# Optimization experiments

Hardware: AMD Instinct MI355X
Metric: run time of the kernel (lower is better)

Reference implementation:

```python
import jax, jax.numpy as jnp
import numpy as np

B, D, NC = 64, 5, 24          # batch, conv output spatial, conv channels
NCELL = D * D                 # 25 objects
FEAT = NC + 2                 # 26 = channels + 2 coords
QDIM = FEAT * NCELL           # 650
PAIR = FEAT * 2 + QDIM        # 702 = g_fc1 in_features
EPS = 1e-5

# cvt_coord(i) = [(i/5 - 2)/2, (i%5 - 2)/2]  (python3 true division)
_i = np.arange(NCELL, dtype=np.float32)
COORDS = jnp.asarray(np.stack([(_i / 5.0 - 2.0) / 2.0, (_i % 5.0 - 2.0) / 2.0], axis=1))  # [25,2]


def _conv_bn(x, w, b, g, beta):
    # Conv2d(stride=2, padding=1) -> ReLU -> BatchNorm2d (training-mode batch stats)
    y = jax.lax.conv_general_dilated(x, w, (2, 2), [(1, 1), (1, 1)],
                                     dimension_numbers=('NCHW', 'OIHW', 'NCHW'))
    y = jax.nn.relu(y + b[None, :, None, None])
    m = y.mean(axis=(0, 2, 3), keepdims=True)
    v = y.var(axis=(0, 2, 3), keepdims=True)  # biased, as torch BN
    return (y - m) * jax.lax.rsqrt(v + EPS) * g[None, :, None, None] + beta[None, :, None, None]


def _cnn(x, conv_w1, conv_w234, conv_b, bn_g, bn_b):
    y = _conv_bn(x, conv_w1, conv_b[0], bn_g[0], bn_b[0])
    for i in range(3):
        y = _conv_bn(y, conv_w234[i], conv_b[i + 1], bn_g[i + 1], bn_b[i + 1])
    return y  # [B,24,5,5]


def setup_inputs() -> dict:
    key = jax.random.key(0)
    ks = jax.random.split(key, 20)
    s = 0.05
    return {
        'img':  jax.random.normal(ks[0], (B, 3, 80, 80), jnp.float32),
        'img2': jax.random.normal(ks[1], (B, 3, 80, 80), jnp.float32),
        'conv_w1':   jax.random.normal(ks[2], (NC, 3, 3, 3), jnp.float32) * s,
        'conv_w234': jax.random.normal(ks[3], (3, NC, NC, 3, 3), jnp.float32) * s,
        'conv_b': jax.random.normal(ks[4], (4, NC), jnp.float32) * s,
        'bn_g':   1.0 + jax.random.normal(ks[5], (4, NC), jnp.float32) * s,
        'bn_b':   jax.random.normal(ks[6], (4, NC), jnp.float32) * s,
        'g_w1':   jax.random.normal(ks[7], (256, PAIR), jnp.float32) * s,
        'g_w234': jax.random.normal(ks[8], (3, 256, 256), jnp.float32) * s,
        'g_b':    jax.random.normal(ks[9], (4, 256), jnp.float32) * s,
        'f_w1':  jax.random.normal(ks[10], (256, 256), jnp.float32) * s,
        'f_b1':  jax.random.normal(ks[11], (256,), jnp.float32) * s,
        'fc2_w': jax.random.normal(ks[12], (256, 256), jnp.float32) * s,
        'fc2_b': jax.random.normal(ks[13], (256,), jnp.float32) * s,
        'fc3_w': jax.random.normal(ks[14], (128, 256), jnp.float32) * s,
        'fc3_b': jax.random.normal(ks[15], (128,), jnp.float32) * s,
    }


def reference(img, img2, conv_w1, conv_w234, conv_b, bn_g, bn_b,
              g_w1, g_w234, g_b, f_w1, f_b1, fc2_w, fc2_b, fc3_w, fc3_b):
    x = _cnn(img, conv_w1, conv_w234, conv_b, bn_g, bn_b)
    x2 = _cnn(img2, conv_w1, conv_w234, conv_b, bn_g, bn_b)

    # [B,24,25] -> [B,25,24] -> concat coords -> [B,25,26]
    coords = jnp.broadcast_to(COORDS[None], (B, NCELL, 2))
    feat = jnp.concatenate([x.reshape(B, NC, NCELL).transpose(0, 2, 1), coords], axis=2)
    feat2 = jnp.concatenate([x2.reshape(B, NC, NCELL).transpose(0, 2, 1), coords], axis=2)
    qst = feat2.reshape(B, QDIM)  # [B,650]

    # x_full[b,a,c] = cat(feat[b,c], feat[b,a], qst[b])  -> [B,25,25,702]
    pair = jnp.concatenate([
        jnp.broadcast_to(feat[:, None, :, :], (B, NCELL, NCELL, FEAT)),
        jnp.broadcast_to(feat[:, :, None, :], (B, NCELL, NCELL, FEAT)),
        jnp.broadcast_to(qst[:, None, None, :], (B, NCELL, NCELL, QDIM)),
    ], axis=-1)

    h = pair.reshape(B * NCELL * NCELL, PAIR)
    h = jax.nn.relu(h @ g_w1.T + g_b[0])
    for i in range(3):
        h = jax.nn.relu(h @ g_w234[i].T + g_b[i + 1])

    x_g = h.reshape(B, NCELL * NCELL, 256).sum(axis=1)  # sum pooling over 625 pairs

    x_f = jax.nn.relu(x_g @ f_w1.T + f_b1)
    y = jax.nn.relu(x_f @ fc2_w.T + fc2_b)
    # F.dropout is identity here (deterministic reference / eval mode)
    y = y @ fc3_w.T + fc3_b                 # [B,128]
    y = jax.nn.softmax(y.reshape(B, 16, 8), axis=2)
    y = jnp.clip(y, 0.001, jnp.max(y))
    return y.reshape(B, 128)
```

## Files before the change

kernel.cpp:

```cpp
#include <hip/hip_runtime.h>

typedef short bf16x8 __attribute__((ext_vector_type(8)));
typedef float f32x4  __attribute__((ext_vector_type(4)));

#define EPSF 1e-5f

#define OFF_P0   0
#define OFF_U    1048576
#define OFF_V    1572864
#define OFF_P1   4915200
#define OFF_SS   6144000
#define OFF_SACC 6144384
#define OFF_Q    6144512
#define OFF_WP   6160896
#define OFF_W1UV 6357504
#define OFF_W1Q  6370816
#define OFF_FW1T 6537216
#define OFF_FC2T 6602752
#define OFF_FC3T 6668288
#define OFF_XG   6701056

__device__ __forceinline__ unsigned short f2bf(float f) {
    union { float f; unsigned u; } cv; cv.f = f;
    const unsigned u = cv.u;
    return (unsigned short)((u + 0x7fffu + ((u >> 16) & 1u)) >> 16);
}
__device__ __forceinline__ float bf2f(unsigned short h) {
    union { unsigned u; float f; } cv; cv.u = (unsigned)h << 16; return cv.f;
}

__global__ __launch_bounds__(256) void k_prep(
    const float* __restrict__ gw1, const float* __restrict__ gw234,
    const float* __restrict__ fw1, const float* __restrict__ fc2w,
    const float* __restrict__ fc3w, float* __restrict__ ws)
{
    int idx = blockIdx.x * 256 + threadIdx.x;
    if (idx < 16384) { ws[OFF_XG + idx] = 0.f; return; }
    idx -= 16384;
    if (idx < 384) {
        if (idx < 96) ws[OFF_SACC + idx] = 0.f;
        else          ws[OFF_U + (idx - 96)] = 0.f;
        return;
    }
    idx -= 384;
    if (idx < 49152) {
        const int isLo = idx >= 24576;
        const int f = isLo ? idx - 24576 : idx;
        const int lane = f & 63;
        const int nt = (f >> 6) & 15;
        const int kb = (f >> 10) & 7;
        const int l  = f >> 13;
        const int o = nt * 16 + (lane & 15);
        const int k = kb * 32 + (lane >> 4) * 8;
        const float* src = gw234 + ((size_t)l * 256 + o) * 256 + k;
        unsigned short* dst = (unsigned short*)(ws + OFF_WP) + (size_t)idx * 8;
        #pragma unroll
        for (int j = 0; j < 8; ++j) {
            const float x = src[j];
            const unsigned short hi = f2bf(x);
            dst[j] = isLo ? f2bf(x - bf2f(hi)) : hi;
        }
        return;
    }
    idx -= 49152;
    if (idx < 13312) {
        const int o = idx & 255, k = idx >> 8;
        ws[OFF_W1UV + idx] = gw1[(size_t)o * 702 + k];
        return;
    }
    idx -= 13312;
    if (idx < 166400) {
        const int o = idx & 255, k = idx >> 8;
        ws[OFF_W1Q + idx] = gw1[(size_t)o * 702 + 52 + k];
        return;
    }
    idx -= 166400;
    if (idx < 65536) { const int o = idx & 255, k = idx >> 8; ws[OFF_FW1T + idx] = fw1[o * 256 + k];  return; }
    idx -= 65536;
    if (idx < 65536) { const int o = idx & 255, k = idx >> 8; ws[OFF_FC2T + idx] = fc2w[o * 256 + k]; return; }
    idx -= 65536;
    if (idx < 32768) { const int o = idx & 127, k = idx >> 7; ws[OFF_FC3T + idx] = fc3w[o * 256 + k]; return; }
}

__global__ __launch_bounds__(256) void k_convF(
    const float* __restrict__ img, const float* __restrict__ img2,
    const float* __restrict__ w, const float* __restrict__ bias,
    float* __restrict__ out, float* __restrict__ sacc)
{
    __shared__ float lds[3*17*82 + 648 + 24];
    __shared__ float lstat[48];
    float* lin   = lds;
    float* lw    = lds + 3*17*82;
    float* lbias = lw + 648;

    const int b  = blockIdx.x / 5;
    const int ty = blockIdx.x % 5;
    const int oy0 = ty * 8;
    const int t = threadIdx.x;

    for (int i = t; i < 648; i += 256) {
        const int co = i % 24, tap = (i / 24) % 9, ci = i / 216;
        lw[i] = w[(co*3 + ci)*9 + tap];
    }
    if (t < 24) lbias[t] = bias[t];
    if (t >= 64 && t < 112) lstat[t - 64] = 0.f;

    const float* src = (b < 64 ? img : img2) + (size_t)(b & 63) * 3 * 6400;
    for (int i = t; i < 3*17*82; i += 256) {
        const int ci = i / (17*82);
        const int r  = i % (17*82);
        const int y  = r / 82, x = r % 82;
        const int gy = 2*oy0 - 1 + y, gx = x - 1;
        float v = 0.f;
        if (gy >= 0 && gy < 80 && gx >= 0 && gx < 80)
            v = src[ci*6400 + gy*80 + gx];
        lin[i] = v;
    }
    __syncthreads();

    const int NWI = 8 * 20 * 24;
    for (int wk = t; wk < NWI; wk += 256) {
        const int co = wk % 24;
        const int pr = wk / 24;
        const int i2 = (pr % 20) * 2;
        const int j  = pr / 20;
        float sA = lbias[co], sB = sA;
        const float* wp = lw + co;
        #pragma unroll
        for (int ci = 0; ci < 3; ++ci) {
            const int base = (ci*17 + 2*j)*82 + 2*i2;
            const float* wc = wp + ci * 216;
            #pragma unroll
            for (int kh = 0; kh < 3; ++kh) {
                const float* lr = lin + base + kh*82;
                const float2 fa = *(const float2*)lr;
                const float2 fb = *(const float2*)(lr + 2);
                const float  fc = lr[4];
                const float w0 = wc[(kh*3 + 0)*24];
                const float w1 = wc[(kh*3 + 1)*24];
                const float w2 = wc[(kh*3 + 2)*24];
                sA += fa.x*w0 + fa.y*w1 + fb.x*w2;
                sB += fb.x*w0 + fb.y*w1 + fc  *w2;
            }
        }
        const float vA = fmaxf(sA, 0.f), vB = fmaxf(sB, 0.f);
        const size_t o = (((size_t)b*24 + co)*40 + oy0 + j)*40 + i2;
        out[o]     = vA;
        out[o + 1] = vB;
        atomicAdd(&lstat[co],      vA + vB);
        atomicAdd(&lstat[24 + co], vA*vA + vB*vB);
    }
    __syncthreads();
    if (t < 48) {
        const int img_i = b >> 6, c = t % 24;
        const int dst = (t < 24) ? (img_i*24 + c) : (48 + img_i*24 + c);
        atomicAdd(&sacc[dst], lstat[t]);
    }
}

__device__ __forceinline__ void convL_body(
    const float* __restrict__ in, const float* __restrict__ ss,
    const float* __restrict__ w, const float* __restrict__ bias,
    float* __restrict__ out, float* __restrict__ sacc,
    float* lds, const int IH, const int IW, const int OH, const int OW,
    const int TH, const int nty)
{
    const int NR = 2*TH + 1, CSTR = IW + 2;
    float* lin = lds;
    float* lw  = lds + 5040;

    const int b  = blockIdx.x / nty;
    const int ty = blockIdx.x % nty;
    const int oy0 = ty * TH;
    const int t = threadIdx.x;

    for (int i = t; i < 5184; i += 256) {
        const int co = i % 24, tap = (i / 24) % 9, ci = i / 216;
        lw[i] = w[(co*24 + ci)*9 + tap];
    }

    const float* sc = ss + (b >> 6) * 48;
    for (int i = t; i < 24 * NR * CSTR; i += 256) {
        const int ci = i / (NR * CSTR);
        const int r  = i % (NR * CSTR);
        const int y  = r / CSTR, x = r % CSTR;
        const int gy = 2*oy0 - 1 + y, gx = x - 1;
        float v = 0.f;
        if (gy >= 0 && gy < IH && gx >= 0 && gx < IW)
            v = in[(((size_t)b*24 + ci)*IH + gy)*IW + gx] * sc[ci] + sc[24 + ci];
        lin[i] = v;
    }
    __syncthreads();

    const int THe = (TH < OH - oy0) ? TH : (OH - oy0);
    const int QPR = (OW + 3) >> 2;
    const int NWI = THe * QPR * 24;
    float ssum = 0.f, ssq = 0.f;
    int myco = 0;
    bool have = false;
    if (t < NWI) {
        const int co = t % 24;
        const int q  = t / 24;
        const int i4 = (q % QPR) * 4;
        const int j  = q / QPR;
        const int n4 = (OW - i4 < 4) ? (OW - i4) : 4;
        float s0 = bias[co], s1 = s0, s2 = s0, s3 = s0;
        const float* wp = lw + co;
        for (int ci = 0; ci < 24; ++ci) {
            const int base = (ci*NR + 2*j)*CSTR + 2*i4;
            const float* wc = wp + ci * 216;
            #pragma unroll
            for (int kh = 0; kh < 3; ++kh) {
                const float* lr = lin + base + kh*CSTR;
                const float2 a0 = *(const float2*)lr;
                const float2 a1 = *(const float2*)(lr + 2);
                const float2 a2 = *(const float2*)(lr + 4);
                const float2 a3 = *(const float2*)(lr + 6);
                const float  a8 = lr[8];
                const float w0 = wc[(kh*3 + 0)*24];
                const float w1 = wc[(kh*3 + 1)*24];
                const float w2 = wc[(kh*3 + 2)*24];
                s0 += a0.x*w0 + a0.y*w1 + a1.x*w2;
                s1 += a1.x*w0 + a1.y*w1 + a2.x*w2;
                s2 += a2.x*w0 + a2.y*w1 + a3.x*w2;
                s3 += a3.x*w0 + a3.y*w1 + a8  *w2;
            }
        }
        const size_t o = (((size_t)b*24 + co)*OH + oy0 + j)*OW + i4;
        const float v0 = fmaxf(s0, 0.f);
        out[o] = v0;  ssum = v0;  ssq = v0*v0;
        if (n4 > 1) { const float v1 = fmaxf(s1, 0.f); out[o+1] = v1; ssum += v1; ssq += v1*v1; }
        if (n4 > 2) { const float v2 = fmaxf(s2, 0.f); out[o+2] = v2; ssum += v2; ssq += v2*v2; }
        if (n4 > 3) { const float v3 = fmaxf(s3, 0.f); out[o+3] = v3; ssum += v3; ssq += v3*v3; }
        myco = co; have = true;
    }
    __syncthreads();
    if (t < 48) lin[t] = 0.f;
    __syncthreads();
    if (have) { atomicAdd(&lin[myco], ssum); atomicAdd(&lin[24 + myco], ssq); }
    __syncthreads();
    if (t < 48) {
        const int img_i = b >> 6, c = t % 24;
        const int dst = (t < 24) ? (img_i*24 + c) : (48 + img_i*24 + c);
        atomicAdd(&sacc[dst], lin[t]);
    }
}

__global__ __launch_bounds__(256) void k_convL2(
    const float* __restrict__ in, const float* __restrict__ ss,
    const float* __restrict__ w, const float* __restrict__ bias,
    float* __restrict__ out, float* __restrict__ sacc)
{
    __shared__ float lds[10224];
    convL_body(in, ss, w, bias, out, sacc, lds, 40, 40, 20, 20, 2, 10);
}
__global__ __launch_bounds__(256) void k_convL3(
    const float* __restrict__ in, const float* __restrict__ ss,
    const float* __restrict__ w, const float* __restrict__ bias,
    float* __restrict__ out, float* __restrict__ sacc)
{
    __shared__ float lds[10224];
    convL_body(in, ss, w, bias, out, sacc, lds, 20, 20, 10, 10, 3, 4);
}
__global__ __launch_bounds__(256) void k_convL4(
    const float* __restrict__ in, const float* __restrict__ ss,
    const float* __restrict__ w, const float* __restrict__ bias,
    float* __restrict__ out, float* __restrict__ sacc)
{
    __shared__ float lds[10224];
    convL_body(in, ss, w, bias, out, sacc, lds, 10, 10, 5, 5, 5, 1);
}

__global__ void k_stats_fin(const float* __restrict__ sacc, const float* __restrict__ g,
                            const float* __restrict__ beta, float* __restrict__ ss, int HW)
{
    const int t = threadIdx.x;
    if (t >= 48) return;
    const int img = t / 24, c = t % 24;
    const float N = 64.f * (float)HW;
    const float mean = sacc[t] / N;
    const float var  = sacc[48 + t] / N - mean*mean;
    const float scale = g[c] * rsqrtf(var + EPSF);
    ss[img*48 + c]      = scale;
    ss[img*48 + 24 + c] = beta[c] - mean * scale;
}

__global__ __launch_bounds__(256) void k_uvq(
    const float* __restrict__ P1, const float* __restrict__ SS4,
    const float* __restrict__ w1uvT, const float* __restrict__ w1qT,
    const float* __restrict__ gb,
    float* __restrict__ Ub, float* __restrict__ Vb, float* __restrict__ Qb)
{
    __shared__ float f[650];
    const int t = threadIdx.x;
    if (blockIdx.x < 1600) {
        const int row = blockIdx.x;
        const int b = row / 25, cell = row % 25;
        if (t < 26) {
            float v;
            if (t < 24)      v = P1[((size_t)(b*24 + t))*25 + cell] * SS4[t] + SS4[24 + t];
            else if (t == 24) v = ((float)cell / 5.f - 2.f) * 0.5f;
            else              v = ((float)(cell % 5) - 2.f) * 0.5f;
            f[t] = v;
        }
        __syncthreads();
        float su = 0.f, sv = 0.f;
        #pragma unroll
        for (int k = 0; k < 26; ++k) {
            su += f[k] * w1uvT[k*256 + t];
            sv += f[k] * w1uvT[(26 + k)*256 + t];
        }
        Ub[(size_t)row*256 + t] = su;
        Vb[(size_t)row*256 + t] = sv;
    } else {
        const int b = blockIdx.x - 1600;
        for (int i = t; i < 650; i += 256) {
            const int cell = i / 26, ff = i % 26;
            float v;
            if (ff < 24)      v = P1[((size_t)((64 + b)*24 + ff))*25 + cell] * SS4[48 + ff] + SS4[72 + ff];
            else if (ff == 24) v = ((float)cell / 5.f - 2.f) * 0.5f;
            else               v = ((float)(cell % 5) - 2.f) * 0.5f;
            f[i] = v;
        }
        __syncthreads();
        float s = gb[t];
        #pragma unroll 10
        for (int k = 0; k < 650; ++k) s += f[k] * w1qT[k*256 + t];
        Qb[b*256 + t] = s;
    }
}

__global__ __launch_bounds__(256, 4) void k_gmlp(
    const float* __restrict__ U, const float* __restrict__ V, const float* __restrict__ Q,
    const unsigned short* __restrict__ WP, const float* __restrict__ gb, float* __restrict__ xg)
{
    __shared__ unsigned short hhi[8192];
    __shared__ unsigned short hlo[8192];
    const int b    = blockIdx.x / 20;
    const int row0 = (blockIdx.x % 20) * 32;
    const int tid  = threadIdx.x;
    const int lane = tid & 63, w = tid >> 6;
    const int w4 = w * 4;

    {
        const int r0 = w * 8;
        const float2* Q2 = (const float2*)(Q + b*256);
        const float2 q0 = Q2[lane], q1 = Q2[64 + lane];
        for (int rr = 0; rr < 8; ++rr) {
            const int row = r0 + rr;
            int p = row0 + row; if (p > 624) p = 624;
            const float2* u2p = (const float2*)(U + ((size_t)(b*25 + p % 25)) * 256);
            const float2* v2p = (const float2*)(V + ((size_t)(b*25 + p / 25)) * 256);
            #pragma unroll
            for (int cc = 0; cc < 2; ++cc) {
                const int cp = cc*64 + lane;
                const float2 u2 = u2p[cp], v2 = v2p[cp];
                const float2 q2 = cc ? q1 : q0;
                const float x0 = fmaxf(u2.x + v2.x + q2.x, 0.f);
                const float x1 = fmaxf(u2.y + v2.y + q2.y, 0.f);
                const unsigned short h0 = f2bf(x0), h1 = f2bf(x1);
                const float l0 = x0 - bf2f(h0), l1 = x1 - bf2f(h1);
                const int byte = (row*512 + cp*4) ^ ((row & 7) << 4);
                *(unsigned*)((char*)hhi + byte) = (unsigned)h0 | ((unsigned)h1 << 16);
                *(unsigned*)((char*)hlo + byte) = (unsigned)f2bf(l0) | ((unsigned)f2bf(l1) << 16);
            }
        }
    }
    __syncthreads();

    const bf16x8* WPB = (const bf16x8*)WP;
    f32x4 acc[2][4];
    #pragma unroll 1
    for (int l = 0; l < 3; ++l) {
        #pragma unroll
        for (int rs = 0; rs < 2; ++rs)
            #pragma unroll
            for (int n = 0; n < 4; ++n) acc[rs][n] = (f32x4)0.f;

        #pragma unroll 1
        for (int kb = 0; kb < 8; ++kb) {
            bf16x8 wh[4], wl[4];
            #pragma unroll
            for (int n = 0; n < 4; ++n) {
                const bf16x8* p = WPB + ((size_t)((l*8 + kb)*16 + w4 + n))*64 + lane;
                wh[n] = p[0]; wl[n] = p[24576];
            }
            bf16x8 ahi[2], alo[2];
            #pragma unroll
            for (int rs = 0; rs < 2; ++rs) {
                const int ar = rs*16 + (lane & 15);
                const int off = (ar*512 + kb*64 + (lane >> 4)*16) ^ ((ar & 7) << 4);
                ahi[rs] = *(const bf16x8*)((char*)hhi + off);
                alo[rs] = *(const bf16x8*)((char*)hlo + off);
            }
            #pragma unroll
            for (int n = 0; n < 4; ++n) {
                #pragma unroll
                for (int rs = 0; rs < 2; ++rs) {
                    acc[rs][n] = __builtin_amdgcn_mfma_f32_16x16x32_bf16(ahi[rs], wh[n], acc[rs][n], 0, 0, 0);
                    acc[rs][n] = __builtin_amdgcn_mfma_f32_16x16x32_bf16(ahi[rs], wl[n], acc[rs][n], 0, 0, 0);
                    acc[rs][n] = __builtin_amdgcn_mfma_f32_16x16x32_bf16(alo[rs], wh[n], acc[rs][n], 0, 0, 0);
                }
            }
        }
        __syncthreads();
        if (l < 2) {
            #pragma unroll
            for (int n = 0; n < 4; ++n) {
                const int col = (w4 + n)*16 + (lane & 15);
                const float bias = gb[(l+1)*256 + col];
                #pragma unroll
                for (int rs = 0; rs < 2; ++rs) {
                    #pragma unroll
                    for (int r = 0; r < 4; ++r) {
                        const int row = rs*16 + 4*(lane >> 4) + r;
                        const float v = fmaxf(acc[rs][n][r] + bias, 0.f);
                        const unsigned short hv = f2bf(v);
                        const float lv = v - bf2f(hv);
                        const int byte = (row*512 + col*2) ^ ((row & 7) << 4);
                        *(unsigned short*)((char*)hhi + byte) = hv;
                        *(unsigned short*)((char*)hlo + byte) = f2bf(lv);
                    }
                }
            }
            __syncthreads();
        } else {
            #pragma unroll
            for (int n = 0; n < 4; ++n) {
                const int col = (w4 + n)*16 + (lane & 15);
                const float bias = gb[3*256 + col];
                float s = 0.f;
                #pragma unroll
                for (int rs = 0; rs < 2; ++rs) {
                    #pragma unroll
                    for (int r = 0; r < 4; ++r) {
                        const int row = rs*16 + 4*(lane >> 4) + r;
                        if (row0 + row < 625) s += fmaxf(acc[rs][n][r] + bias, 0.f);
                    }
                }
                s += __shfl_xor(s, 16);
                s += __shfl_xor(s, 32);
                if (lane < 16) atomicAdd(&xg[b*256 + col], s);
            }
        }
    }
}

__global__ __launch_bounds__(256) void k_head(
    const float* __restrict__ XG, const float* __restrict__ fw1T, const float* __restrict__ fb1,
    const float* __restrict__ fc2T, const float* __restrict__ fc2b,
    const float* __restrict__ fc3T, const float* __restrict__ fc3b, float* __restrict__ out)
{
    __shared__ float xa[256], xb[256], ys[128];
    const int b = blockIdx.x, t = threadIdx.x;
    xa[t] = XG[b*256 + t];
    __syncthreads();
    float s = fb1[t];
    #pragma unroll 8
    for (int k = 0; k < 256; ++k) s += xa[k] * fw1T[k*256 + t];
    xb[t] = fmaxf(s, 0.f);
    __syncthreads();
    s = fc2b[t];
    #pragma unroll 8
    for (int k = 0; k < 256; ++k) s += xb[k] * fc2T[k*256 + t];
    xa[t] = fmaxf(s, 0.f);
    __syncthreads();
    if (t < 128) {
        s = fc3b[t];
        #pragma unroll 8
        for (int k = 0; k < 256; ++k) s += xa[k] * fc3T[k*128 + t];
        ys[t] = s;
    }
    __syncthreads();
    if (t < 16) {
        float m = ys[t*8];
        #pragma unroll
        for (int i = 1; i < 8; ++i) m = fmaxf(m, ys[t*8 + i]);
        float e[8], sum = 0.f;
        #pragma unroll
        for (int i = 0; i < 8; ++i) { e[i] = expf(ys[t*8 + i] - m); sum += e[i]; }
        const float inv = 1.f / sum;
        #pragma unroll
        for (int i = 0; i < 8; ++i) out[b*128 + t*8 + i] = fmaxf(e[i]*inv, 0.001f);
    }
}

extern "C" void kernel_launch(void* const* d_in, const int* in_sizes, int n_in,
                              void* d_out, int out_size, void* d_ws, size_t ws_size,
                              hipStream_t stream)
{
    const float* img   = (const float*)d_in[0];
    const float* img2  = (const float*)d_in[1];
    const float* cw1   = (const float*)d_in[2];
    const float* cw234 = (const float*)d_in[3];
    const float* cb    = (const float*)d_in[4];
    const float* bng   = (const float*)d_in[5];
    const float* bnb   = (const float*)d_in[6];
    const float* gw1   = (const float*)d_in[7];
    const float* gw234 = (const float*)d_in[8];
    const float* gb    = (const float*)d_in[9];
    const float* fw1   = (const float*)d_in[10];
    const float* fb1   = (const float*)d_in[11];
    const float* fc2w  = (const float*)d_in[12];
    const float* fc2b  = (const float*)d_in[13];
    const float* fc3w  = (const float*)d_in[14];
    const float* fc3b  = (const float*)d_in[15];

    float* ws = (float*)d_ws;
    float* P0 = ws + OFF_P0;  float* P1 = ws + OFF_P1;   float* SS  = ws + OFF_SS;
    float* SA1 = ws + OFF_SACC;
    float* SA2 = ws + OFF_U;
    float* SA3 = ws + OFF_U + 96;
    float* SA4 = ws + OFF_U + 192;
    float* Ub = ws + OFF_U;   float* Vb  = ws + OFF_V;   float* Qb = ws + OFF_Q;
    unsigned short* WP = (unsigned short*)(ws + OFF_WP);
    float* W1UV = ws + OFF_W1UV; float* W1Q = ws + OFF_W1Q;
    float* FW1T = ws + OFF_FW1T; float* FC2T = ws + OFF_FC2T; float* FC3T = ws + OFF_FC3T;
    float* XG = ws + OFF_XG;
    float* out = (float*)d_out;

    hipLaunchKernelGGL(k_prep, dim3(1600), dim3(256), 0, stream, gw1, gw234, fw1, fc2w, fc3w, ws);

    hipLaunchKernelGGL(k_convF, dim3(640), dim3(256), 0, stream, img, img2, cw1, cb, P0, SA1);
    hipLaunchKernelGGL(k_stats_fin, dim3(1), dim3(64), 0, stream, SA1, bng, bnb, SS, 1600);
    hipLaunchKernelGGL(k_convL2, dim3(1280), dim3(256), 0, stream,
                       P0, SS, cw234, cb + 24, P1, SA2);
    hipLaunchKernelGGL(k_stats_fin, dim3(1), dim3(64), 0, stream, SA2, bng + 24, bnb + 24, SS + 96, 400);
    hipLaunchKernelGGL(k_convL3, dim3(512), dim3(256), 0, stream,
                       P1, SS + 96, cw234 + 5184, cb + 48, P0, SA3);
    hipLaunchKernelGGL(k_stats_fin, dim3(1), dim3(64), 0, stream, SA3, bng + 48, bnb + 48, SS + 192, 100);
    hipLaunchKernelGGL(k_convL4, dim3(128), dim3(256), 0, stream,
                       P0, SS + 192, cw234 + 10368, cb + 72, P1, SA4);
    hipLaunchKernelGGL(k_stats_fin, dim3(1), dim3(64), 0, stream, SA4, bng + 72, bnb + 72, SS + 288, 25);

    hipLaunchKernelGGL(k_uvq, dim3(1664), dim3(256), 0, stream,
                       P1, SS + 288, W1UV, W1Q, gb, Ub, Vb, Qb);

    hipLaunchKernelGGL(k_gmlp, dim3(1280), dim3(256), 0, stream, Ub, Vb, Qb, WP, gb, XG);

    hipLaunchKernelGGL(k_head, dim3(64), dim3(256), 0, stream,
                       XG, FW1T, fb1, FC2T, fc2b, FC3T, fc3b, out);
}
```

Measured before the change: 272.0 us.

## Process two row tiles per conv block and double-buffer MFMA weight loads

Conv layers 2 and 3 now have each block loop over two output row tiles. The transposed weight staging into LDS is paid once per two tiles, and the grids are halved to match. Separately, the g-MLP inner k-loop is unrolled by two with ping-pong weight registers, so the next k-block's global weight fragments are prefetched while the current MFMAs run. The costs are fewer blocks (less parallelism) for the convs and higher register pressure in the MLP kernel.

Result: slower. 284.2 us (+4.5%).

```diff
diff --git a/kernel.cpp b/kernel.cpp
--- a/kernel.cpp
+++ b/kernel.cpp
@@ -163,78 +163,82 @@
     const float* __restrict__ w, const float* __restrict__ bias,
     float* __restrict__ out, float* __restrict__ sacc,
     float* lds, const int IH, const int IW, const int OH, const int OW,
-    const int TH, const int nty)
+    const int TH, const int ntyB, const int NTILES)
 {
     const int NR = 2*TH + 1, CSTR = IW + 2;
     float* lin = lds;
     float* lw  = lds + 5040;
 
-    const int b  = blockIdx.x / nty;
-    const int ty = blockIdx.x % nty;
-    const int oy0 = ty * TH;
+    const int b   = blockIdx.x / ntyB;
+    const int tyB = (blockIdx.x % ntyB) * NTILES;
     const int t = threadIdx.x;
 
     for (int i = t; i < 5184; i += 256) {
         const int co = i % 24, tap = (i / 24) % 9, ci = i / 216;
         lw[i] = w[(co*24 + ci)*9 + tap];
     }
-
     const float* sc = ss + (b >> 6) * 48;
-    for (int i = t; i < 24 * NR * CSTR; i += 256) {
-        const int ci = i / (NR * CSTR);
-        const int r  = i % (NR * CSTR);
-        const int y  = r / CSTR, x = r % CSTR;
-        const int gy = 2*oy0 - 1 + y, gx = x - 1;
-        float v = 0.f;
-        if (gy >= 0 && gy < IH && gx >= 0 && gx < IW)
-            v = in[(((size_t)b*24 + ci)*IH + gy)*IW + gx] * sc[ci] + sc[24 + ci];
-        lin[i] = v;
-    }
-    __syncthreads();
-
-    const int THe = (TH < OH - oy0) ? TH : (OH - oy0);
-    const int QPR = (OW + 3) >> 2;
-    const int NWI = THe * QPR * 24;
+
     float ssum = 0.f, ssq = 0.f;
-    int myco = 0;
+    const int myco = t % 24;
     bool have = false;
-    if (t < NWI) {
-        const int co = t % 24;
-        const int q  = t / 24;
-        const int i4 = (q % QPR) * 4;
-        const int j  = q / QPR;
-        const int n4 = (OW - i4 < 4) ? (OW - i4) : 4;
-        float s0 = bias[co], s1 = s0, s2 = s0, s3 = s0;
-        const float* wp = lw + co;
-        for (int ci = 0; ci < 24; ++ci) {
-            const int base = (ci*NR + 2*j)*CSTR + 2*i4;
-            const float* wc = wp + ci * 216;
-            #pragma unroll
-            for (int kh = 0; kh < 3; ++kh) {
-                const float* lr = lin + base + kh*CSTR;
-                const float2 a0 = *(const float2*)lr;
-                const float2 a1 = *(const float2*)(lr + 2);
-                const float2 a2 = *(const float2*)(lr + 4);
-                const float2 a3 = *(const float2*)(lr + 6);
-                const float  a8 = lr[8];
-                const float w0 = wc[(kh*3 + 0)*24];
-                const float w1 = wc[(kh*3 + 1)*24];
-                const float w2 = wc[(kh*3 + 2)*24];
-                s0 += a0.x*w0 + a0.y*w1 + a1.x*w2;
-                s1 += a1.x*w0 + a1.y*w1 + a2.x*w2;
-                s2 += a2.x*w0 + a2.y*w1 + a3.x*w2;
-                s3 += a3.x*w0 + a3.y*w1 + a8  *w2;
-            }
-        }
-        const size_t o = (((size_t)b*24 + co)*OH + oy0 + j)*OW + i4;
-        const float v0 = fmaxf(s0, 0.f);
-        out[o] = v0;  ssum = v0;  ssq = v0*v0;
-        if (n4 > 1) { const float v1 = fmaxf(s1, 0.f); out[o+1] = v1; ssum += v1; ssq += v1*v1; }
-        if (n4 > 2) { const float v2 = fmaxf(s2, 0.f); out[o+2] = v2; ssum += v2; ssq += v2*v2; }
-        if (n4 > 3) { const float v3 = fmaxf(s3, 0.f); out[o+3] = v3; ssum += v3; ssq += v3*v3; }
-        myco = co; have = true;
-    }
-    __syncthreads();
+
+    for (int tile = 0; tile < NTILES; ++tile) {
+        const int oy0 = (tyB + tile) * TH;
+        for (int i = t; i < 24 * NR * CSTR; i += 256) {
+            const int ci = i / (NR * CSTR);
+            const int r  = i % (NR * CSTR);
+            const int y  = r / CSTR, x = r % CSTR;
+            const int gy = 2*oy0 - 1 + y, gx = x - 1;
+            float v = 0.f;
+            if (gy >= 0 && gy < IH && gx >= 0 && gx < IW)
+                v = in[(((size_t)b*24 + ci)*IH + gy)*IW + gx] * sc[ci] + sc[24 + ci];
+            lin[i] = v;
+        }
+        __syncthreads();
+
+        const int THe = (TH < OH - oy0) ? TH : (OH - oy0);
+        const int QPR = (OW + 3) >> 2;
+        const int NWI = THe * QPR * 24;
+        if (t < NWI) {
+            const int co = myco;
+            const int q  = t / 24;
+            const int i4 = (q % QPR) * 4;
+            const int j  = q / QPR;
+            const int n4 = (OW - i4 < 4) ? (OW - i4) : 4;
+            float s0 = bias[co], s1 = s0, s2 = s0, s3 = s0;
+            const float* wp = lw + co;
+            for (int ci = 0; ci < 24; ++ci) {
+                const int base = (ci*NR + 2*j)*CSTR + 2*i4;
+                const float* wc = wp + ci * 216;
+                #pragma unroll
+                for (int kh = 0; kh < 3; ++kh) {
+                    const float* lr = lin + base + kh*CSTR;
+                    const float2 a0 = *(const float2*)lr;
+                    const float2 a1 = *(const float2*)(lr + 2);
+                    const float2 a2 = *(const float2*)(lr + 4);
+                    const float2 a3 = *(const float2*)(lr + 6);
+                    const float  a8 = lr[8];
+                    const float w0 = wc[(kh*3 + 0)*24];
+                    const float w1 = wc[(kh*3 + 1)*24];
+                    const float w2 = wc[(kh*3 + 2)*24];
+                    s0 += a0.x*w0 + a0.y*w1 + a1.x*w2;
+                    s1 += a1.x*w0 + a1.y*w1 + a2.x*w2;
+                    s2 += a2.x*w0 + a2.y*w1 + a3.x*w2;
+                    s3 += a3.x*w0 + a3.y*w1 + a8  *w2;
+                }
+            }
+            const size_t o = (((size_t)b*24 + co)*OH + oy0 + j)*OW + i4;
+            const float v0 = fmaxf(s0, 0.f);
+            out[o] = v0;  ssum += v0;  ssq += v0*v0;
+            if (n4 > 1) { const float v1 = fmaxf(s1, 0.f); out[o+1] = v1; ssum += v1; ssq += v1*v1; }
+            if (n4 > 2) { const float v2 = fmaxf(s2, 0.f); out[o+2] = v2; ssum += v2; ssq += v2*v2; }
+            if (n4 > 3) { const float v3 = fmaxf(s3, 0.f); out[o+3] = v3; ssum += v3; ssq += v3*v3; }
+            have = true;
+        }
+        __syncthreads();
+    }
+
     if (t < 48) lin[t] = 0.f;
     __syncthreads();
     if (have) { atomicAdd(&lin[myco], ssum); atomicAdd(&lin[24 + myco], ssq); }
@@ -252,7 +256,7 @@
     float* __restrict__ out, float* __restrict__ sacc)
 {
     __shared__ float lds[10224];
-    convL_body(in, ss, w, bias, out, sacc, lds, 40, 40, 20, 20, 2, 10);
+    convL_body(in, ss, w, bias, out, sacc, lds, 40, 40, 20, 20, 2, 5, 2);
 }
 __global__ __launch_bounds__(256) void k_convL3(
     const float* __restrict__ in, const float* __restrict__ ss,
@@ -260,7 +264,7 @@
     float* __restrict__ out, float* __restrict__ sacc)
 {
     __shared__ float lds[10224];
-    convL_body(in, ss, w, bias, out, sacc, lds, 20, 20, 10, 10, 3, 4);
+    convL_body(in, ss, w, bias, out, sacc, lds, 20, 20, 10, 10, 3, 2, 2);
 }
 __global__ __launch_bounds__(256) void k_convL4(
     const float* __restrict__ in, const float* __restrict__ ss,
@@ -268,7 +272,7 @@
     float* __restrict__ out, float* __restrict__ sacc)
 {
     __shared__ float lds[10224];
-    convL_body(in, ss, w, bias, out, sacc, lds, 10, 10, 5, 5, 5, 1);
+    convL_body(in, ss, w, bias, out, sacc, lds, 10, 10, 5, 5, 5, 1, 1);
 }
 
 __global__ void k_stats_fin(const float* __restrict__ sacc, const float* __restrict__ g,
@@ -377,29 +381,64 @@
             #pragma unroll
             for (int n = 0; n < 4; ++n) acc[rs][n] = (f32x4)0.f;
 
+        bf16x8 wah[4], wal[4], wbh[4], wbl[4];
+        #pragma unroll
+        for (int n = 0; n < 4; ++n) {
+            const bf16x8* p = WPB + ((size_t)((l*8 + 0)*16 + w4 + n))*64 + lane;
+            wah[n] = p[0]; wal[n] = p[24576];
+        }
+
         #pragma unroll 1
-        for (int kb = 0; kb < 8; ++kb) {
-            bf16x8 wh[4], wl[4];
+        for (int kb2 = 0; kb2 < 4; ++kb2) {
+            const int kb = kb2 * 2;
             #pragma unroll
             for (int n = 0; n < 4; ++n) {
-                const bf16x8* p = WPB + ((size_t)((l*8 + kb)*16 + w4 + n))*64 + lane;
-                wh[n] = p[0]; wl[n] = p[24576];
-            }
-            bf16x8 ahi[2], alo[2];
-            #pragma unroll
-            for (int rs = 0; rs < 2; ++rs) {
-                const int ar = rs*16 + (lane & 15);
-                const int off = (ar*512 + kb*64 + (lane >> 4)*16) ^ ((ar & 7) << 4);
-                ahi[rs] = *(const bf16x8*)((char*)hhi + off);
-                alo[rs] = *(const bf16x8*)((char*)hlo + off);
-            }
-            #pragma unroll
-            for (int n = 0; n < 4; ++n) {
+                const bf16x8* p = WPB + ((size_t)((l*8 + kb + 1)*16 + w4 + n))*64 + lane;
+                wbh[n] = p[0]; wbl[n] = p[24576];
+            }
+            {
+                bf16x8 ahi[2], alo[2];
                 #pragma unroll
                 for (int rs = 0; rs < 2; ++rs) {
-                    acc[rs][n] = __builtin_amdgcn_mfma_f32_16x16x32_bf16(ahi[rs], wh[n], acc[rs][n], 0, 0, 0);
-                    acc[rs][n] = __builtin_amdgcn_mfma_f32_16x16x32_bf16(ahi[rs], wl[n], acc[rs][n], 0, 0, 0);
-                    acc[rs][n] = __builtin_amdgcn_mfma_f32_16x16x32_bf16(alo[rs], wh[n], acc[rs][n], 0, 0, 0);
+                    const int ar = rs*16 + (lane & 15);
+                    const int off = (ar*512 + kb*64 + (lane >> 4)*16) ^ ((ar & 7) << 4);
+                    ahi[rs] = *(const bf16x8*)((char*)hhi + off);
+                    alo[rs] = *(const bf16x8*)((char*)hlo + off);
+                }
+                #pragma unroll
+                for (int n = 0; n < 4; ++n) {
+                    #pragma unroll
+                    for (int rs = 0; rs < 2; ++rs) {
+                        acc[rs][n] = __builtin_amdgcn_mfma_f32_16x16x32_bf16(ahi[rs], wah[n], acc[rs][n], 0, 0, 0);
+                        acc[rs][n] = __builtin_amdgcn_mfma_f32_16x16x32_bf16(ahi[rs], wal[n], acc[rs][n], 0, 0, 0);
+                        acc[rs][n] = __builtin_amdgcn_mfma_f32_16x16x32_bf16(alo[rs], wah[n], acc[rs][n], 0, 0, 0);
+                    }
+                }
+            }
+            if (kb2 < 3) {
+                #pragma unroll
+                for (int n = 0; n < 4; ++n) {
+                    const bf16x8* p = WPB + ((size_t)((l*8 + kb + 2)*16 + w4 + n))*64 + lane;
+                    wah[n] = p[0]; wal[n] = p[24576];
+                }
+            }
+            {
+                bf16x8 ahi[2], alo[2];
+                #pragma unroll
+                for (int rs = 0; rs < 2; ++rs) {
+                    const int ar = rs*16 + (lane & 15);
+                    const int off = (ar*512 + (kb + 1)*64 + (lane >> 4)*16) ^ ((ar & 7) << 4);
+                    ahi[rs] = *(const bf16x8*)((char*)hhi + off);
+                    alo[rs] = *(const bf16x8*)((char*)hlo + off);
+                }
+                #pragma unroll
+                for (int n = 0; n < 4; ++n) {
+                    #pragma unroll
+                    for (int rs = 0; rs < 2; ++rs) {
+                        acc[rs][n] = __builtin_amdgcn_mfma_f32_16x16x32_bf16(ahi[rs], wbh[n], acc[rs][n], 0, 0, 0);
+                        acc[rs][n] = __builtin_amdgcn_mfma_f32_16x16x32_bf16(ahi[rs], wbl[n], acc[rs][n], 0, 0, 0);
+                        acc[rs][n] = __builtin_amdgcn_mfma_f32_16x16x32_bf16(alo[rs], wbh[n], acc[rs][n], 0, 0, 0);
+                    }
                 }
             }
         }
@@ -523,10 +562,10 @@
 
     hipLaunchKernelGGL(k_convF, dim3(640), dim3(256), 0, stream, img, img2, cw1, cb, P0, SA1);
     hipLaunchKernelGGL(k_stats_fin, dim3(1), dim3(64), 0, stream, SA1, bng, bnb, SS, 1600);
-    hipLaunchKernelGGL(k_convL2, dim3(1280), dim3(256), 0, stream,
+    hipLaunchKernelGGL(k_convL2, dim3(640), dim3(256), 0, stream,
                        P0, SS, cw234, cb + 24, P1, SA2);
     hipLaunchKernelGGL(k_stats_fin, dim3(1), dim3(64), 0, stream, SA2, bng + 24, bnb + 24, SS + 96, 400);
-    hipLaunchKernelGGL(k_convL3, dim3(512), dim3(256), 0, stream,
+    hipLaunchKernelGGL(k_convL3, dim3(256), dim3(256), 0, stream,
                        P1, SS + 96, cw234 + 5184, cb + 48, P0, SA3);
     hipLaunchKernelGGL(k_stats_fin, dim3(1), dim3(64), 0, stream, SA3, bng + 48, bnb + 48, SS + 192, 100);
     hipLaunchKernelGGL(k_convL4, dim3(128), dim3(256), 0, stream,
```
